# Kernel optimization log

Hardware: AMD Instinct MI355X
Metric: run time of the kernel (lower is better)

## Reference

```python
import jax, jax.numpy as jnp
import numpy as np

B, N = 8192, 4096
OUT_DIM = 32


def setup_inputs() -> dict:
    key = jax.random.key(0)
    k_rr, k_drop, k_w1, k_b1, k_w2, k_b2 = jax.random.split(key, 6)
    rr = jax.random.uniform(k_rr, (B, N), dtype=jnp.float32, minval=0.4, maxval=1.4)
    drop = jax.random.uniform(k_drop, (B, N)) < 0.3
    rr = jnp.where(drop, 0.0, rr)
    # projection MLP params (Linear(6,16) -> ReLU -> Dropout(eval: identity) -> Linear(16,32))
    w1 = jax.random.normal(k_w1, (6, 16), dtype=jnp.float32) * (1.0 / np.sqrt(6))
    b1 = jax.random.normal(k_b1, (16,), dtype=jnp.float32) * 0.01
    w2 = jax.random.normal(k_w2, (16, OUT_DIM), dtype=jnp.float32) * (1.0 / np.sqrt(16))
    b2 = jax.random.normal(k_b2, (OUT_DIM,), dtype=jnp.float32) * 0.01
    return {"rr_intervals": rr, "w1": w1, "b1": b1, "w2": w2, "b2": b2}


def _hrv_features(rr):
    # rr: (B, N) float32, zero-padded. Faithful to the per-row torch loop, vectorized.
    dt = rr.dtype
    mask = rr > 0                                   # (B, N)
    cnt = jnp.sum(mask, axis=1)                     # (B,) int
    cntf = cnt.astype(dt)
    # masked mean / unbiased std (torch.std default ddof=1)
    denom_m = jnp.maximum(cntf, 1.0)
    mean_rr = jnp.sum(jnp.where(mask, rr, 0.0), axis=1) / denom_m
    dev = jnp.where(mask, rr - mean_rr[:, None], 0.0)
    var = jnp.sum(dev * dev, axis=1) / jnp.maximum(cntf - 1.0, 1.0)
    sdnn = jnp.sqrt(var)
    # compact valid entries to the front (stable -> preserves order), so diffs
    # match torch.diff(rr[rr > 0])
    order = jnp.argsort(jnp.logical_not(mask), axis=1, stable=True)  # (B, N)
    compact = jnp.take_along_axis(rr, order, axis=1)                  # (B, N)
    diffs = compact[:, 1:] - compact[:, :-1]                          # (B, N-1)
    dmask = jnp.arange(N - 1)[None, :] < (cnt - 1)[:, None]           # valid diffs
    ndiff = jnp.maximum(cntf - 1.0, 1.0)
    rmssd = jnp.sqrt(jnp.sum(jnp.where(dmask, diffs * diffs, 0.0), axis=1) / ndiff)
    nn50 = jnp.sum(((jnp.abs(diffs) > 0.05) & dmask).astype(dt), axis=1)
    pnn50 = nn50 / ndiff
    hr = 60.0 / jnp.maximum(mean_rr, 1e-12)
    cv = sdnn / jnp.maximum(mean_rr, 1e-12)
    feats = jnp.stack([mean_rr, sdnn, rmssd, pnn50, hr, cv], axis=1)  # (B, 6)
    feats = jnp.where((cnt > 1)[:, None], feats, 0.0)
    # per-column batch normalization, applied only where column max > 0
    col_max = jnp.max(feats, axis=0)
    col_mean = jnp.mean(feats, axis=0)
    col_std = jnp.std(feats, axis=0, ddof=1)
    normed = (feats - col_mean[None, :]) / (col_std[None, :] + 1e-8)
    feats = jnp.where((col_max > 0)[None, :], normed, feats)
    return feats


def reference(rr_intervals, w1, b1, w2, b2):
    feats = _hrv_features(rr_intervals)                 # (B, 6)
    h = jax.nn.relu(feats @ w1 + b1)                    # (B, 16); dropout in eval = identity
    return h @ w2 + b2                                  # (B, OUT_DIM)
```

## Files before the change

kernel.cpp:

```cpp
#include <hip/hip_runtime.h>
#include <math.h>

#define BATCH 8192
#define NLEN 4096
#define THREADS 256
#define PER_THREAD (NLEN / THREADS)

__global__ __launch_bounds__(THREADS) void hrv_feats_kernel(
    const float* __restrict__ rr, float* __restrict__ feats) {
    __shared__ float sh_last[THREADS];
    __shared__ unsigned char sh_has[THREADS];
    __shared__ double sh_sum[4], sh_sumsq[4], sh_sumd2[4];
    __shared__ int sh_cnt[4], sh_nn50[4];

    const int row = blockIdx.x;
    const int t = threadIdx.x;
    const float* r = rr + (size_t)row * NLEN + t * PER_THREAD;

    float x[PER_THREAD];
    float4* xv = reinterpret_cast<float4*>(x);
    const float4* rv = reinterpret_cast<const float4*>(r);
#pragma unroll
    for (int i = 0; i < PER_THREAD / 4; ++i) xv[i] = rv[i];

    float sum = 0.f, sumsq = 0.f, sumd2 = 0.f;
    int cnt = 0, nn50 = 0;
    float first = 0.f, last = 0.f;
    int has = 0;
#pragma unroll
    for (int i = 0; i < PER_THREAD; ++i) {
        float v = x[i];
        if (v > 0.f) {
            sum += v;
            sumsq += v * v;
            ++cnt;
            if (has) {
                float d = v - last;
                sumd2 += d * d;
                nn50 += (fabsf(d) > 0.05f) ? 1 : 0;
            } else {
                first = v;
                has = 1;
            }
            last = v;
        }
    }
    sh_last[t] = last;
    sh_has[t] = (unsigned char)has;
    __syncthreads();
    if (has && t > 0) {
        for (int j = t - 1; j >= 0; --j) {
            if (sh_has[j]) {
                float d = first - sh_last[j];
                sumd2 += d * d;
                nn50 += (fabsf(d) > 0.05f) ? 1 : 0;
                break;
            }
        }
    }

    double dsum = sum, dsumsq = sumsq, dsumd2 = sumd2;
    int icnt = cnt, inn = nn50;
#pragma unroll
    for (int off = 32; off > 0; off >>= 1) {
        dsum += __shfl_down(dsum, off, 64);
        dsumsq += __shfl_down(dsumsq, off, 64);
        dsumd2 += __shfl_down(dsumd2, off, 64);
        icnt += __shfl_down(icnt, off, 64);
        inn += __shfl_down(inn, off, 64);
    }
    const int wave = t >> 6;
    if ((t & 63) == 0) {
        sh_sum[wave] = dsum;
        sh_sumsq[wave] = dsumsq;
        sh_sumd2[wave] = dsumd2;
        sh_cnt[wave] = icnt;
        sh_nn50[wave] = inn;
    }
    __syncthreads();
    if (t == 0) {
        double S = 0, S2 = 0, D2 = 0;
        int C = 0, NN = 0;
        for (int w = 0; w < 4; ++w) {
            S += sh_sum[w];
            S2 += sh_sumsq[w];
            D2 += sh_sumd2[w];
            C += sh_cnt[w];
            NN += sh_nn50[w];
        }
        const float cntf = (float)C;
        const float denom_m = fmaxf(cntf, 1.f);
        const float mean = (float)(S / (double)denom_m);
        const float varsum = (float)(S2 - (double)C * (double)mean * (double)mean);
        const float denom_v = fmaxf(cntf - 1.f, 1.f);
        const float sdnn = sqrtf(fmaxf(varsum / denom_v, 0.f));
        const float rmssd = sqrtf(fmaxf((float)(D2 / (double)denom_v), 0.f));
        const float pnn50 = (float)NN / denom_v;
        const float hr = 60.f / fmaxf(mean, 1e-12f);
        const float cv = sdnn / fmaxf(mean, 1e-12f);
        float f0 = mean, f1 = sdnn, f2 = rmssd, f3 = pnn50, f4 = hr, f5 = cv;
        if (C <= 1) { f0 = f1 = f2 = f3 = f4 = f5 = 0.f; }
        float* o = feats + row * 6;
        o[0] = f0; o[1] = f1; o[2] = f2;
        o[3] = f3; o[4] = f4; o[5] = f5;
    }
}

__global__ __launch_bounds__(256) void stats_mlp_kernel(
    const float* __restrict__ feats,
    const float* __restrict__ w1, const float* __restrict__ b1,
    const float* __restrict__ w2, const float* __restrict__ b2,
    float* __restrict__ out) {
    __shared__ double sh_s[4][6], sh_s2[4][6];
    __shared__ float sh_m[4][6];
    __shared__ float sh_stats[18];

    const int t = threadIdx.x;
    double s[6] = {0, 0, 0, 0, 0, 0};
    double s2[6] = {0, 0, 0, 0, 0, 0};
    float mx[6] = {-INFINITY, -INFINITY, -INFINITY, -INFINITY, -INFINITY, -INFINITY};

#pragma unroll 4
    for (int i = t; i < BATCH; i += 256) {
        const float* fp = feats + i * 6;
#pragma unroll
        for (int c = 0; c < 6; ++c) {
            float f = fp[c];
            s[c] += (double)f;
            s2[c] += (double)f * (double)f;
            mx[c] = fmaxf(mx[c], f);
        }
    }
#pragma unroll
    for (int off = 32; off; off >>= 1) {
#pragma unroll
        for (int c = 0; c < 6; ++c) {
            s[c] += __shfl_down(s[c], off, 64);
            s2[c] += __shfl_down(s2[c], off, 64);
            mx[c] = fmaxf(mx[c], __shfl_down(mx[c], off, 64));
        }
    }
    if ((t & 63) == 0) {
        const int w = t >> 6;
#pragma unroll
        for (int c = 0; c < 6; ++c) {
            sh_s[w][c] = s[c];
            sh_s2[w][c] = s2[c];
            sh_m[w][c] = mx[c];
        }
    }
    __syncthreads();
    if (t < 6) {
        double S = 0, S2 = 0;
        float M = -INFINITY;
        for (int w = 0; w < 4; ++w) {
            S += sh_s[w][t];
            S2 += sh_s2[w][t];
            M = fmaxf(M, sh_m[w][t]);
        }
        const double meanb = S / (double)BATCH;
        double var = (S2 - (double)BATCH * meanb * meanb) / (double)(BATCH - 1);
        if (var < 0.0) var = 0.0;
        sh_stats[t] = (float)meanb;
        sh_stats[6 + t] = (float)sqrt(var);
        sh_stats[12 + t] = M;
    }
    __syncthreads();

    const int row = blockIdx.x * 256 + t;
    const float* fp = feats + row * 6;
    float f[6];
#pragma unroll
    for (int c = 0; c < 6; ++c) {
        float v = fp[c];
        if (sh_stats[12 + c] > 0.f) v = (v - sh_stats[c]) / (sh_stats[6 + c] + 1e-8f);
        f[c] = v;
    }
    float h[16];
#pragma unroll
    for (int j = 0; j < 16; ++j) {
        float a = b1[j];
#pragma unroll
        for (int c = 0; c < 6; ++c) a = fmaf(f[c], w1[c * 16 + j], a);
        h[j] = fmaxf(a, 0.f);
    }
    float o[32];
#pragma unroll
    for (int k = 0; k < 32; ++k) o[k] = b2[k];
#pragma unroll
    for (int j = 0; j < 16; ++j) {
        const float hj = h[j];
#pragma unroll
        for (int k = 0; k < 32; ++k) o[k] = fmaf(hj, w2[j * 32 + k], o[k]);
    }
    float4* ov = reinterpret_cast<float4*>(out + (size_t)row * 32);
    const float4* op = reinterpret_cast<const float4*>(o);
#pragma unroll
    for (int i = 0; i < 8; ++i) ov[i] = op[i];
}

extern "C" void kernel_launch(void* const* d_in, const int* in_sizes, int n_in,
                              void* d_out, int out_size, void* d_ws, size_t ws_size,
                              hipStream_t stream) {
    const float* rr = (const float*)d_in[0];
    const float* w1 = (const float*)d_in[1];
    const float* b1 = (const float*)d_in[2];
    const float* w2 = (const float*)d_in[3];
    const float* b2 = (const float*)d_in[4];
    float* out = (float*)d_out;
    float* feats = (float*)d_ws;

    hrv_feats_kernel<<<BATCH, THREADS, 0, stream>>>(rr, feats);
    stats_mlp_kernel<<<BATCH / 256, THREADS, 0, stream>>>(feats, w1, b1, w2, b2, out);
}
```

Baseline: 40.70 us.

## Accumulate batch column statistics via binned atomics in feature kernel

The feature kernel now atomically accumulates per-column sum, sum of squares and max into 64 bins indexed by row. The second kernel reduces those bins with one wave instead of having every one of its 32 blocks re-read all 8192x6 features redundantly. This removes the redundant per-block full-batch stats pass but adds a memset launch and 18 atomics per row, including double-precision atomics. The max uses uint atomicMax on float bits, which gives the correct order only for non-negative values; that holds here because the features are non-negative.

```diff
diff --git a/kernel.cpp b/kernel.cpp
--- a/kernel.cpp
+++ b/kernel.cpp
@@ -5,9 +5,20 @@
 #define NLEN 4096
 #define THREADS 256
 #define PER_THREAD (NLEN / THREADS)
+#define NBIN 64
+
+#define OFF_S   (BATCH * 6 * 4)
+#define OFF_S2  (OFF_S + 6 * NBIN * 8)
+#define OFF_MX  (OFF_S2 + 6 * NBIN * 8)
+#define BIN_BYTES (6 * NBIN * (8 + 8 + 4))
 
 __global__ __launch_bounds__(THREADS) void hrv_feats_kernel(
-    const float* __restrict__ rr, float* __restrict__ feats) {
+    const float* __restrict__ rr, unsigned char* __restrict__ wsb) {
+    float* feats = reinterpret_cast<float*>(wsb);
+    double* s_bins = reinterpret_cast<double*>(wsb + OFF_S);
+    double* s2_bins = reinterpret_cast<double*>(wsb + OFF_S2);
+    unsigned int* mx_bins = reinterpret_cast<unsigned int*>(wsb + OFF_MX);
+
     __shared__ float sh_last[THREADS];
     __shared__ unsigned char sh_has[THREADS];
     __shared__ double sh_sum[4], sh_sumsq[4], sh_sumd2[4];
@@ -98,72 +109,64 @@
         const float pnn50 = (float)NN / denom_v;
         const float hr = 60.f / fmaxf(mean, 1e-12f);
         const float cv = sdnn / fmaxf(mean, 1e-12f);
-        float f0 = mean, f1 = sdnn, f2 = rmssd, f3 = pnn50, f4 = hr, f5 = cv;
-        if (C <= 1) { f0 = f1 = f2 = f3 = f4 = f5 = 0.f; }
+        float f[6] = {mean, sdnn, rmssd, pnn50, hr, cv};
+        if (C <= 1) {
+#pragma unroll
+            for (int c = 0; c < 6; ++c) f[c] = 0.f;
+        }
         float* o = feats + row * 6;
-        o[0] = f0; o[1] = f1; o[2] = f2;
-        o[3] = f3; o[4] = f4; o[5] = f5;
+        const int bin = row & (NBIN - 1);
+#pragma unroll
+        for (int c = 0; c < 6; ++c) {
+            o[c] = f[c];
+            atomicAdd(&s_bins[c * NBIN + bin], (double)f[c]);
+            atomicAdd(&s2_bins[c * NBIN + bin], (double)f[c] * (double)f[c]);
+            atomicMax(&mx_bins[c * NBIN + bin], __float_as_uint(f[c]));
+        }
     }
 }
 
 __global__ __launch_bounds__(256) void stats_mlp_kernel(
-    const float* __restrict__ feats,
+    const unsigned char* __restrict__ wsb,
     const float* __restrict__ w1, const float* __restrict__ b1,
     const float* __restrict__ w2, const float* __restrict__ b2,
     float* __restrict__ out) {
-    __shared__ double sh_s[4][6], sh_s2[4][6];
-    __shared__ float sh_m[4][6];
+    const float* feats = reinterpret_cast<const float*>(wsb);
+    const double* s_bins = reinterpret_cast<const double*>(wsb + OFF_S);
+    const double* s2_bins = reinterpret_cast<const double*>(wsb + OFF_S2);
+    const unsigned int* mx_bins =
+        reinterpret_cast<const unsigned int*>(wsb + OFF_MX);
+
     __shared__ float sh_stats[18];
-
     const int t = threadIdx.x;
-    double s[6] = {0, 0, 0, 0, 0, 0};
-    double s2[6] = {0, 0, 0, 0, 0, 0};
-    float mx[6] = {-INFINITY, -INFINITY, -INFINITY, -INFINITY, -INFINITY, -INFINITY};
-
-#pragma unroll 4
-    for (int i = t; i < BATCH; i += 256) {
-        const float* fp = feats + i * 6;
+
+    if (t < 64) {
+        double S[6], S2[6];
+        float M[6];
 #pragma unroll
         for (int c = 0; c < 6; ++c) {
-            float f = fp[c];
-            s[c] += (double)f;
-            s2[c] += (double)f * (double)f;
-            mx[c] = fmaxf(mx[c], f);
-        }
-    }
-#pragma unroll
-    for (int off = 32; off; off >>= 1) {
-#pragma unroll
-        for (int c = 0; c < 6; ++c) {
-            s[c] += __shfl_down(s[c], off, 64);
-            s2[c] += __shfl_down(s2[c], off, 64);
-            mx[c] = fmaxf(mx[c], __shfl_down(mx[c], off, 64));
-        }
-    }
-    if ((t & 63) == 0) {
-        const int w = t >> 6;
-#pragma unroll
-        for (int c = 0; c < 6; ++c) {
-            sh_s[w][c] = s[c];
-            sh_s2[w][c] = s2[c];
-            sh_m[w][c] = mx[c];
-        }
-    }
-    __syncthreads();
-    if (t < 6) {
-        double S = 0, S2 = 0;
-        float M = -INFINITY;
-        for (int w = 0; w < 4; ++w) {
-            S += sh_s[w][t];
-            S2 += sh_s2[w][t];
-            M = fmaxf(M, sh_m[w][t]);
-        }
-        const double meanb = S / (double)BATCH;
-        double var = (S2 - (double)BATCH * meanb * meanb) / (double)(BATCH - 1);
-        if (var < 0.0) var = 0.0;
-        sh_stats[t] = (float)meanb;
-        sh_stats[6 + t] = (float)sqrt(var);
-        sh_stats[12 + t] = M;
+            S[c] = s_bins[c * NBIN + t];
+            S2[c] = s2_bins[c * NBIN + t];
+            M[c] = __uint_as_float(mx_bins[c * NBIN + t]);
+        }
+#pragma unroll
+        for (int off = 32; off; off >>= 1) {
+#pragma unroll
+            for (int c = 0; c < 6; ++c) {
+                S[c] += __shfl_xor(S[c], off, 64);
+                S2[c] += __shfl_xor(S2[c], off, 64);
+                M[c] = fmaxf(M[c], __shfl_xor(M[c], off, 64));
+            }
+        }
+        if (t < 6) {
+            const double meanb = S[t] / (double)BATCH;
+            double var =
+                (S2[t] - (double)BATCH * meanb * meanb) / (double)(BATCH - 1);
+            if (var < 0.0) var = 0.0;
+            sh_stats[t] = (float)meanb;
+            sh_stats[6 + t] = (float)sqrt(var);
+            sh_stats[12 + t] = M[t];
+        }
     }
     __syncthreads();
 
@@ -173,7 +176,8 @@
 #pragma unroll
     for (int c = 0; c < 6; ++c) {
         float v = fp[c];
-        if (sh_stats[12 + c] > 0.f) v = (v - sh_stats[c]) / (sh_stats[6 + c] + 1e-8f);
+        if (sh_stats[12 + c] > 0.f)
+            v = (v - sh_stats[c]) / (sh_stats[6 + c] + 1e-8f);
         f[c] = v;
     }
     float h[16];
@@ -208,8 +212,9 @@
     const float* w2 = (const float*)d_in[3];
     const float* b2 = (const float*)d_in[4];
     float* out = (float*)d_out;
-    float* feats = (float*)d_ws;
-
-    hrv_feats_kernel<<<BATCH, THREADS, 0, stream>>>(rr, feats);
-    stats_mlp_kernel<<<BATCH / 256, THREADS, 0, stream>>>(feats, w1, b1, w2, b2, out);
+    unsigned char* wsb = (unsigned char*)d_ws;
+
+    hipMemsetAsync(wsb + OFF_S, 0, BIN_BYTES, stream);
+    hrv_feats_kernel<<<BATCH, THREADS, 0, stream>>>(rr, wsb);
+    stats_mlp_kernel<<<BATCH / 256, THREADS, 0, stream>>>(wsb, w1, b1, w2, b2, out);
 }
```

After: 70.33 us. 1.73x slower.

## Store features column-major, vectorize stats reads, stage MLP weights in LDS, remap rows

Applied to the files above, without the earlier changes.

The feature buffer moves from row-major (B,6) to column-major (6,B), so the stats kernel can read each column with coalesced float4 loads, each thread issuing a batch of independent loads. MLP weights and biases are staged once in shared memory rather than read from global memory in the inner loops. Block-to-row mapping in the feature kernel is permuted so consecutive blocks touch rows spread across the batch, presumably to spread memory channel traffic. The main cost is the 128 MB streaming read in the first kernel, which these changes mostly leave untouched.

```diff
diff --git a/kernel.cpp b/kernel.cpp
--- a/kernel.cpp
+++ b/kernel.cpp
@@ -13,7 +13,7 @@
     __shared__ double sh_sum[4], sh_sumsq[4], sh_sumd2[4];
     __shared__ int sh_cnt[4], sh_nn50[4];
 
-    const int row = blockIdx.x;
+    const int row = ((blockIdx.x & 7) << 10) | (blockIdx.x >> 3);
     const int t = threadIdx.x;
     const float* r = rr + (size_t)row * NLEN + t * PER_THREAD;
 
@@ -98,11 +98,13 @@
         const float pnn50 = (float)NN / denom_v;
         const float hr = 60.f / fmaxf(mean, 1e-12f);
         const float cv = sdnn / fmaxf(mean, 1e-12f);
-        float f0 = mean, f1 = sdnn, f2 = rmssd, f3 = pnn50, f4 = hr, f5 = cv;
-        if (C <= 1) { f0 = f1 = f2 = f3 = f4 = f5 = 0.f; }
-        float* o = feats + row * 6;
-        o[0] = f0; o[1] = f1; o[2] = f2;
-        o[3] = f3; o[4] = f4; o[5] = f5;
+        float f[6] = {mean, sdnn, rmssd, pnn50, hr, cv};
+        if (C <= 1) {
+#pragma unroll
+            for (int c = 0; c < 6; ++c) f[c] = 0.f;
+        }
+#pragma unroll
+        for (int c = 0; c < 6; ++c) feats[c * BATCH + row] = f[c];
     }
 }
 
@@ -111,24 +113,48 @@
     const float* __restrict__ w1, const float* __restrict__ b1,
     const float* __restrict__ w2, const float* __restrict__ b2,
     float* __restrict__ out) {
+    __shared__ float sh_w[656];
     __shared__ double sh_s[4][6], sh_s2[4][6];
     __shared__ float sh_m[4][6];
     __shared__ float sh_stats[18];
 
     const int t = threadIdx.x;
-    double s[6] = {0, 0, 0, 0, 0, 0};
-    double s2[6] = {0, 0, 0, 0, 0, 0};
-    float mx[6] = {-INFINITY, -INFINITY, -INFINITY, -INFINITY, -INFINITY, -INFINITY};
-
-#pragma unroll 4
-    for (int i = t; i < BATCH; i += 256) {
-        const float* fp = feats + i * 6;
-#pragma unroll
-        for (int c = 0; c < 6; ++c) {
-            float f = fp[c];
-            s[c] += (double)f;
-            s2[c] += (double)f * (double)f;
-            mx[c] = fmaxf(mx[c], f);
+
+    for (int i = t; i < 656; i += 256) {
+        float v;
+        if (i < 96) v = w1[i];
+        else if (i < 112) v = b1[i - 96];
+        else if (i < 624) v = w2[i - 112];
+        else v = b2[i - 624];
+        sh_w[i] = v;
+    }
+
+    double s[6], s2[6];
+    float mx[6];
+#pragma unroll
+    for (int c = 0; c < 6; ++c) { s[c] = 0.0; s2[c] = 0.0; mx[c] = -INFINITY; }
+
+#pragma unroll
+    for (int cp = 0; cp < 3; ++cp) {
+        const float4* c0 =
+            reinterpret_cast<const float4*>(feats + (2 * cp) * BATCH);
+        const float4* c1 =
+            reinterpret_cast<const float4*>(feats + (2 * cp + 1) * BATCH);
+        float4 buf[16];
+#pragma unroll
+        for (int k = 0; k < 8; ++k) buf[k] = c0[t + k * 256];
+#pragma unroll
+        for (int k = 0; k < 8; ++k) buf[8 + k] = c1[t + k * 256];
+#pragma unroll
+        for (int k = 0; k < 16; ++k) {
+            const int c = 2 * cp + (k >> 3);
+            const float f[4] = {buf[k].x, buf[k].y, buf[k].z, buf[k].w};
+#pragma unroll
+            for (int e = 0; e < 4; ++e) {
+                s[c] += (double)f[e];
+                s2[c] += (double)f[e] * (double)f[e];
+                mx[c] = fmaxf(mx[c], f[e]);
+            }
         }
     }
 #pragma unroll
@@ -168,30 +194,30 @@
     __syncthreads();
 
     const int row = blockIdx.x * 256 + t;
-    const float* fp = feats + row * 6;
     float f[6];
 #pragma unroll
     for (int c = 0; c < 6; ++c) {
-        float v = fp[c];
-        if (sh_stats[12 + c] > 0.f) v = (v - sh_stats[c]) / (sh_stats[6 + c] + 1e-8f);
+        float v = feats[c * BATCH + row];
+        if (sh_stats[12 + c] > 0.f)
+            v = (v - sh_stats[c]) / (sh_stats[6 + c] + 1e-8f);
         f[c] = v;
     }
     float h[16];
 #pragma unroll
     for (int j = 0; j < 16; ++j) {
-        float a = b1[j];
-#pragma unroll
-        for (int c = 0; c < 6; ++c) a = fmaf(f[c], w1[c * 16 + j], a);
+        float a = sh_w[96 + j];
+#pragma unroll
+        for (int c = 0; c < 6; ++c) a = fmaf(f[c], sh_w[c * 16 + j], a);
         h[j] = fmaxf(a, 0.f);
     }
     float o[32];
 #pragma unroll
-    for (int k = 0; k < 32; ++k) o[k] = b2[k];
+    for (int k = 0; k < 32; ++k) o[k] = sh_w[624 + k];
 #pragma unroll
     for (int j = 0; j < 16; ++j) {
         const float hj = h[j];
 #pragma unroll
-        for (int k = 0; k < 32; ++k) o[k] = fmaf(hj, w2[j * 32 + k], o[k]);
+        for (int k = 0; k < 32; ++k) o[k] = fmaf(hj, sh_w[112 + j * 32 + k], o[k]);
     }
     float4* ov = reinterpret_cast<float4*>(out + (size_t)row * 32);
     const float4* op = reinterpret_cast<const float4*>(o);
```

Measured after the change: 39.22 us (median of 2 runs). 3.6% less time.
